# Optimization experiments

Measured on AMD Instinct MI355X. Metric: run time of the kernel, lower is better.

## Reference

```python
import jax, jax.numpy as jnp
import numpy as np

BS, SEQ, D_MODEL, N_HEADS = 4, 2048, 1024, 16
D_HEAD = D_MODEL // N_HEADS


def setup_inputs() -> dict:
    key = jax.random.key(0)
    ks = jax.random.split(key, 12)
    s = 1.0 / np.sqrt(D_MODEL)
    return {
        "Q": jax.random.normal(ks[0], (BS, SEQ, D_MODEL), jnp.float32),
        "K": jax.random.normal(ks[1], (BS, SEQ, D_MODEL), jnp.float32),
        "V": jax.random.normal(ks[2], (BS, SEQ, D_MODEL), jnp.float32),
        "mask": jax.random.randint(ks[3], (BS, 1, 1, SEQ), 0, 2, jnp.int32),
        "Wq": jax.random.normal(ks[4], (D_MODEL, D_MODEL), jnp.float32) * s,
        "bq": jnp.zeros((D_MODEL,), jnp.float32),
        "Wk": jax.random.normal(ks[5], (D_MODEL, D_MODEL), jnp.float32) * s,
        "bk": jnp.zeros((D_MODEL,), jnp.float32),
        "Wv": jax.random.normal(ks[6], (D_MODEL, D_MODEL), jnp.float32) * s,
        "bv": jnp.zeros((D_MODEL,), jnp.float32),
        "Wo": jax.random.normal(ks[7], (D_MODEL, D_MODEL), jnp.float32) * s,
        "bo": jnp.zeros((D_MODEL,), jnp.float32),
    }


def _split_heads(x):
    # (b, s, d_model) -> (b, h, s, d_head)
    b, s, _ = x.shape
    return x.reshape(b, s, N_HEADS, D_HEAD).transpose(0, 2, 1, 3)


def reference(Q, K, V, mask, Wq, bq, Wk, bk, Wv, bv, Wo, bo):
    q = _split_heads(Q @ Wq.T + bq)
    k = _split_heads(K @ Wk.T + bk)
    v = _split_heads(V @ Wv.T + bv)
    # (b, h, sq, sk) score matrix, scaled by sqrt(d_head)
    scores = jnp.einsum("bhqd,bhkd->bhqk", q, k) / np.sqrt(D_HEAD).astype(np.float32)
    scores = jnp.where(mask == 0, jnp.float32(-1e9), scores)
    attn = jax.nn.softmax(scores, axis=-1)
    ctx = jnp.einsum("bhqk,bhkd->bhqd", attn, v)
    b, h, s, d = ctx.shape
    ctx = ctx.transpose(0, 2, 1, 3).reshape(b, s, h * d)
    return ctx @ Wo.T + bo
```

## Files before the change

kernel.cpp:

```cpp
#include <hip/hip_runtime.h>


typedef __attribute__((ext_vector_type(8))) unsigned short us8;
typedef __attribute__((ext_vector_type(4))) unsigned short us4;
typedef __attribute__((ext_vector_type(4))) int i4;
typedef __attribute__((ext_vector_type(4))) float f4;
typedef __attribute__((ext_vector_type(4))) float f32x4;
typedef __attribute__((ext_vector_type(8))) __bf16 bf16x8;
typedef __attribute__((ext_vector_type(2))) unsigned u32x2;
typedef __attribute__((ext_vector_type(4))) unsigned u32x4;

#define DEV static __device__ __forceinline__

DEV unsigned short f2bf(float f){
  unsigned u = __builtin_bit_cast(unsigned, f);
  u = (u + 0x7fffu + ((u >> 16) & 1u)) >> 16;
  return (unsigned short)u;
}

DEV bf16x8 ld_frag(const unsigned short* p){
  return __builtin_bit_cast(bf16x8, *(const us8*)p);
}

DEV void gll16(const unsigned short* gsrc, unsigned short* ldst){
  __builtin_amdgcn_global_load_lds(
      (const __attribute__((address_space(1))) unsigned int*)gsrc,
      (__attribute__((address_space(3))) unsigned int*)ldst, 16, 0, 0);
}

DEV us8 ld_cvt_f32x8(const float* p){
  f4 v0 = *(const f4*)p;
  f4 v1 = *(const f4*)(p + 4);
  unsigned d0, d1, d2, d3;
  asm("v_cvt_pk_bf16_f32 %0, %1, %2" : "=v"(d0) : "v"(v0[0]), "v"(v0[1]));
  asm("v_cvt_pk_bf16_f32 %0, %1, %2" : "=v"(d1) : "v"(v0[2]), "v"(v0[3]));
  asm("v_cvt_pk_bf16_f32 %0, %1, %2" : "=v"(d2) : "v"(v1[0]), "v"(v1[1]));
  asm("v_cvt_pk_bf16_f32 %0, %1, %2" : "=v"(d3) : "v"(v1[2]), "v"(v1[3]));
  u32x4 u = {d0, d1, d2, d3};
  return __builtin_bit_cast(us8, u);
}

__global__ void cvt_bf16x4(const float* __restrict__ w0, const float* __restrict__ w1,
                           const float* __restrict__ w2, const float* __restrict__ w3,
                           unsigned short* __restrict__ o0, unsigned short* __restrict__ o1,
                           unsigned short* __restrict__ o2, unsigned short* __restrict__ o3)
{
  const int z = blockIdx.y;
  const float* src = (z == 0) ? w0 : (z == 1) ? w1 : (z == 2) ? w2 : w3;
  unsigned short* dst = (z == 0) ? o0 : (z == 1) ? o1 : (z == 2) ? o2 : o3;
  int i = blockIdx.x * 256 + threadIdx.x;
  *(us8*)(dst + (size_t)i * 8) = ld_cvt_f32x8(src + (size_t)i * 8);
}

__global__ __launch_bounds__(256) void mask_scan(
    const int* __restrict__ mask, int* __restrict__ idx, int* __restrict__ nk)
{
  const int b = blockIdx.x, t = threadIdx.x;
  __shared__ int sc[256];
  int m[8]; int c = 0;
#pragma unroll
  for(int r = 0; r < 8; ++r){ m[r] = mask[b * 2048 + t * 8 + r]; c += (m[r] != 0); }
  sc[t] = c;
  __syncthreads();
  for(int s = 1; s < 256; s <<= 1){
    int v = (t >= s) ? sc[t - s] : 0;
    __syncthreads();
    sc[t] += v;
    __syncthreads();
  }
  int pos = sc[t] - c;
  int total = sc[255];
#pragma unroll
  for(int r = 0; r < 8; ++r) if(m[r]) idx[b * 2048 + pos++] = t * 8 + r;
  int pend = (total + 127) & ~127;
  for(int p = total + t; p < pend; p += 256) idx[b * 2048 + p] = 0;
  if(t == 0) nk[b] = total;
}

__global__ __launch_bounds__(256) void qkv_proj(
    const float* __restrict__ Qf, const float* __restrict__ Kf, const float* __restrict__ Vf,
    const unsigned short* __restrict__ Wqb, const unsigned short* __restrict__ Wkb,
    const unsigned short* __restrict__ Wvb,
    const float* __restrict__ bq, const float* __restrict__ bk, const float* __restrict__ bv,
    unsigned short* __restrict__ qs, unsigned short* __restrict__ ksc,
    unsigned short* __restrict__ vTc, float qscale,
    const int* __restrict__ gidx, const int* __restrict__ nkarr)
{
  __shared__ __align__(16) unsigned short As[128 * 64];
  __shared__ __align__(16) unsigned short Bs[128 * 64];
  const int tid = threadIdx.x;
  const int x = blockIdx.x, z = blockIdx.y >> 3, ny = blockIdx.y & 7;
  const int w = tid >> 6, l = tid & 63, g = l >> 4, l15 = l & 15;
  const int wm = w >> 1, wn = w & 1;
  const int xsw = ((l & 7) ^ (l >> 3)) << 3;
  const int ch = tid & 7, srow = tid >> 3;

  int ia[4];
  int gb = 0;
  if(z >= 1){
    gb = (x * 128) >> 11;
    const int j0 = (x * 128) & 2047;
    if(j0 >= ((nkarr[gb] + 127) & ~127)) return;
#pragma unroll
    for(int i = 0; i < 4; ++i)
      ia[i] = gidx[gb * 2048 + j0 + srow + i * 32];
  }

  const float*          Af32 = (z == 0) ? Qf : Kf;
  const unsigned short* Wb   = (z == 0) ? Wqb : Wkb;

  f32x4 acc[4][4];
#pragma unroll
  for(int a = 0; a < 4; ++a)
#pragma unroll
    for(int b = 0; b < 4; ++b) acc[a][b] = (f32x4){0.f,0.f,0.f,0.f};

  for(int kt = 0; kt < 16; ++kt){
    __syncthreads();
    if(z < 2){
#pragma unroll
      for(int i = 0; i < 4; ++i){
        int row = srow + i * 32;
        const float* src = (z == 1)
          ? Af32 + ((size_t)gb * 2048 + ia[i]) * 1024 + kt * 64 + ch * 8
          : Af32 + (size_t)(x * 128 + row) * 1024 + kt * 64 + ch * 8;
        us8 va = ld_cvt_f32x8(src);
        *(us8*)&As[row * 64 + ((ch * 8) ^ ((row & 7) << 3))] = va;
      }
#pragma unroll
      for(int j = 0; j < 4; ++j)
        gll16(Wb + (size_t)(ny * 128 + (w << 5) + (j << 3) + (l >> 3)) * 1024 + kt * 64 + xsw,
              &Bs[((w << 5) + (j << 3)) << 6]);
    } else {
#pragma unroll
      for(int j = 0; j < 4; ++j)
        gll16(Wvb + (size_t)(ny * 128 + (w << 5) + (j << 3) + (l >> 3)) * 1024 + kt * 64 + xsw,
              &As[((w << 5) + (j << 3)) << 6]);
#pragma unroll
      for(int i = 0; i < 4; ++i){
        int row = srow + i * 32;
        const float* src = Vf + ((size_t)gb * 2048 + ia[i]) * 1024 + kt * 64 + ch * 8;
        us8 vb = ld_cvt_f32x8(src);
        *(us8*)&Bs[row * 64 + ((ch * 8) ^ ((row & 7) << 3))] = vb;
      }
    }
    asm volatile("s_waitcnt vmcnt(0)" ::: "memory");
    __syncthreads();
#pragma unroll
    for(int kk = 0; kk < 2; ++kk){
      bf16x8 af[4], bg[4];
#pragma unroll
      for(int mi = 0; mi < 4; ++mi){
        int row = wm * 64 + mi * 16 + l15;
        af[mi] = ld_frag(&As[row * 64 + ((kk * 32 + g * 8) ^ ((row & 7) << 3))]);
      }
#pragma unroll
      for(int ni = 0; ni < 4; ++ni){
        int row = wn * 64 + ni * 16 + l15;
        bg[ni] = ld_frag(&Bs[row * 64 + ((kk * 32 + g * 8) ^ ((row & 7) << 3))]);
      }
#pragma unroll
      for(int mi = 0; mi < 4; ++mi)
#pragma unroll
        for(int ni = 0; ni < 4; ++ni)
          acc[mi][ni] = __builtin_amdgcn_mfma_f32_16x16x32_bf16(af[mi], bg[ni], acc[mi][ni], 0, 0, 0);
    }
  }

  if(z < 2){
    const float scale = (z == 0) ? qscale : 1.0f;
    const float* bias = (z == 0) ? bq : bk;
    unsigned short* out = (z == 0) ? qs : ksc;
#pragma unroll
    for(int mi = 0; mi < 4; ++mi)
#pragma unroll
      for(int ni = 0; ni < 4; ++ni){
        int gmb = x * 128 + wm * 64 + mi * 16 + g * 4;
        int gn  = ny * 128 + wn * 64 + ni * 16 + l15;
#pragma unroll
        for(int r = 0; r < 4; ++r){
          int gm = gmb + r;
          float v = (acc[mi][ni][r] + bias[gn]) * scale;
          int b = gm >> 11, s = gm & 2047, h = gn >> 6, dh = gn & 63;
          out[(size_t)(((b << 4) + h) * 2048 + s) * 64 + dh] = f2bf(v);
        }
      }
  } else {
#pragma unroll
    for(int mi = 0; mi < 4; ++mi)
#pragma unroll
      for(int ni = 0; ni < 4; ++ni){
        int gmb = ny * 128 + wm * 64 + mi * 16 + g * 4;
        int gn  = x * 128 + wn * 64 + ni * 16 + l15;
#pragma unroll
        for(int r = 0; r < 4; ++r){
          int gm = gmb + r;
          float v = acc[mi][ni][r] + bv[gm];
          int h = gm >> 6, dh = gm & 63, b = gn >> 11, s = gn & 2047;
          vTc[(size_t)(((b << 4) + h) * 64 + dh) * 2048 + s] = f2bf(v);
        }
      }
  }
}

__global__ __launch_bounds__(256) void gemm_out(
    const unsigned short* __restrict__ Ap, const unsigned short* __restrict__ Bp,
    const float* __restrict__ bias, float* __restrict__ outp, int K)
{
  __shared__ __align__(16) unsigned short As[128 * 64];
  __shared__ __align__(16) unsigned short Bs[128 * 64];
  const int tid = threadIdx.x;
  const int gy = blockIdx.x, gx = blockIdx.y;
  const int w = tid >> 6, l = tid & 63, g = l >> 4, l15 = l & 15;
  const int wm = w >> 1, wn = w & 1;
  const int xsw = ((l & 7) ^ (l >> 3)) << 3;

  f32x4 acc[4][4];
#pragma unroll
  for(int a = 0; a < 4; ++a)
#pragma unroll
    for(int b = 0; b < 4; ++b) acc[a][b] = (f32x4){0.f,0.f,0.f,0.f};

  const int nkt = K >> 6;
  for(int kt = 0; kt < nkt; ++kt){
    __syncthreads();
#pragma unroll
    for(int j = 0; j < 4; ++j)
      gll16(Ap + (size_t)(gy * 128 + (w << 5) + (j << 3) + (l >> 3)) * K + kt * 64 + xsw,
            &As[((w << 5) + (j << 3)) << 6]);
#pragma unroll
    for(int j = 0; j < 4; ++j)
      gll16(Bp + (size_t)(gx * 128 + (w << 5) + (j << 3) + (l >> 3)) * K + kt * 64 + xsw,
            &Bs[((w << 5) + (j << 3)) << 6]);
    asm volatile("s_waitcnt vmcnt(0)" ::: "memory");
    __syncthreads();
#pragma unroll
    for(int kk = 0; kk < 2; ++kk){
      bf16x8 af[4], bg[4];
#pragma unroll
      for(int mi = 0; mi < 4; ++mi){
        int row = wm * 64 + mi * 16 + l15;
        af[mi] = ld_frag(&As[row * 64 + ((kk * 32 + g * 8) ^ ((row & 7) << 3))]);
      }
#pragma unroll
      for(int ni = 0; ni < 4; ++ni){
        int row = wn * 64 + ni * 16 + l15;
        bg[ni] = ld_frag(&Bs[row * 64 + ((kk * 32 + g * 8) ^ ((row & 7) << 3))]);
      }
#pragma unroll
      for(int mi = 0; mi < 4; ++mi)
#pragma unroll
        for(int ni = 0; ni < 4; ++ni)
          acc[mi][ni] = __builtin_amdgcn_mfma_f32_16x16x32_bf16(af[mi], bg[ni], acc[mi][ni], 0, 0, 0);
    }
  }

#pragma unroll
  for(int mi = 0; mi < 4; ++mi)
#pragma unroll
    for(int ni = 0; ni < 4; ++ni){
      int gmb = gy * 128 + wm * 64 + mi * 16 + g * 4;
      int gn  = gx * 128 + wn * 64 + ni * 16 + l15;
#pragma unroll
      for(int r = 0; r < 4; ++r)
        outp[(size_t)(gmb + r) * 1024 + gn] = acc[mi][ni][r] + bias[gn];
    }
}

__global__ __launch_bounds__(256) void attn_kernel(
    const unsigned short* __restrict__ q, const unsigned short* __restrict__ ksc,
    const unsigned short* __restrict__ vTc, const int* __restrict__ nk,
    unsigned short* __restrict__ ctx)
{
  __shared__ __align__(16) unsigned short KsB[2][64 * 64];
  __shared__ __align__(16) unsigned short VtB[2][64 * 64];
  __shared__ __align__(16) unsigned short Ps[4][16 * 64];

  const int bh = blockIdx.x;
  const int qt = blockIdx.y;
  const int b  = bh >> 4, h = bh & 15;
  const int tid = threadIdx.x;
  const int w = tid >> 6, l = tid & 63, g = l >> 4, l15 = l & 15;
  const int rl = l >> 3, c8 = l & 7;

  const int nkb = nk[b];
  const int nt = (nkb + 63) >> 6;

  const unsigned short* qbase = q + ((size_t)(bh * 2048 + qt * 64 + w * 16 + l15)) * 64;
  bf16x8 bq[2];
  bq[0] = ld_frag(qbase + g * 8);
  bq[1] = ld_frag(qbase + 32 + g * 8);

  const unsigned short* kbase = ksc + (size_t)bh * 2048 * 64;
  const unsigned short* vbase = vTc + (size_t)bh * 64 * 2048;

  const unsigned short* kg0 = kbase + (size_t)(w * 16 + rl) * 64 + c8 * 8;
  const unsigned short* vg0 = vbase + (size_t)(w * 16 + rl) * 2048 + c8 * 8;
  const int lo0 = (w * 16 + rl) * 64 + ((c8 ^ rl) << 3);
  const int lo1 = lo0 + 8 * 64;

  us8 kr0, kr1, vr0, vr1;
#define LOAD_T(kt_) do{                                        \
    kr0 = *(const us8*)(kg0 + (size_t)(kt_) * 4096);           \
    kr1 = *(const us8*)(kg0 + (size_t)(kt_) * 4096 + 512);     \
    vr0 = *(const us8*)(vg0 + (size_t)(kt_) * 64);             \
    vr1 = *(const us8*)(vg0 + (size_t)(kt_) * 64 + 8 * 2048);  \
  }while(0)
#define WRITE_T(bb_) do{                                       \
    *(us8*)&KsB[bb_][lo0] = kr0;                               \
    *(us8*)&KsB[bb_][lo1] = kr1;                               \
    *(us8*)&VtB[bb_][lo0] = vr0;                               \
    *(us8*)&VtB[bb_][lo1] = vr1;                               \
  }while(0)

  f32x4 acc[4];
#pragma unroll
  for(int mi = 0; mi < 4; ++mi) acc[mi] = (f32x4){0.f,0.f,0.f,0.f};
  float ll = 0.f;

  LOAD_T(0);
  WRITE_T(0);
  __syncthreads();

  for(int kt = 0; kt < nt; ++kt){
    const int bb = kt & 1;
    if(kt + 1 < nt) LOAD_T(kt + 1);

    f32x4 sa[4];
#pragma unroll
    for(int mi = 0; mi < 4; ++mi) sa[mi] = (f32x4){0.f,0.f,0.f,0.f};
    __builtin_amdgcn_s_setprio(1);
#pragma unroll
    for(int kk = 0; kk < 2; ++kk){
#pragma unroll
      for(int mi = 0; mi < 4; ++mi){
        int row = mi * 16 + l15;
        bf16x8 af = ld_frag(&KsB[bb][row * 64 + ((kk * 32 + g * 8) ^ ((row & 7) << 3))]);
        sa[mi] = __builtin_amdgcn_mfma_f32_16x16x32_bf16(af, bq[kk], sa[mi], 0, 0, 0);
      }
    }
    __builtin_amdgcn_s_setprio(0);

    float p[4][4];
    if((kt + 1) * 64 <= nkb){
#pragma unroll
      for(int mi = 0; mi < 4; ++mi)
#pragma unroll
        for(int r = 0; r < 4; ++r){
          p[mi][r] = __builtin_amdgcn_exp2f(sa[mi][r]);
          ll += p[mi][r];
        }
    } else {
      int kb0 = kt * 64 + g * 4;
#pragma unroll
      for(int mi = 0; mi < 4; ++mi)
#pragma unroll
        for(int r = 0; r < 4; ++r){
          float e = __builtin_amdgcn_exp2f(sa[mi][r]);
          p[mi][r] = (kb0 + mi * 16 + r < nkb) ? e : 0.f;
          ll += p[mi][r];
        }
    }

#pragma unroll
    for(int mi = 0; mi < 4; ++mi){
      unsigned d0, d1;
      asm("v_cvt_pk_bf16_f32 %0, %1, %2" : "=v"(d0) : "v"(p[mi][0]), "v"(p[mi][1]));
      asm("v_cvt_pk_bf16_f32 %0, %1, %2" : "=v"(d1) : "v"(p[mi][2]), "v"(p[mi][3]));
      u32x2 dd = {d0, d1};
      *(u32x2*)&Ps[w][l15 * 64 + ((mi * 16 + g * 4) ^ ((l15 & 7) << 3))] = dd;
    }

    __builtin_amdgcn_s_setprio(1);
#pragma unroll
    for(int kk = 0; kk < 2; ++kk){
      bf16x8 pb = ld_frag(&Ps[w][l15 * 64 + ((kk * 32 + g * 8) ^ ((l15 & 7) << 3))]);
#pragma unroll
      for(int mi = 0; mi < 4; ++mi){
        int row = mi * 16 + l15;
        bf16x8 av = ld_frag(&VtB[bb][row * 64 + ((kk * 32 + g * 8) ^ ((row & 7) << 3))]);
        acc[mi] = __builtin_amdgcn_mfma_f32_16x16x32_bf16(av, pb, acc[mi], 0, 0, 0);
      }
    }
    __builtin_amdgcn_s_setprio(0);

    if(kt + 1 < nt) WRITE_T(bb ^ 1);
    __syncthreads();
  }

  ll += __shfl_xor(ll, 16);
  ll += __shfl_xor(ll, 32);
  float inv = 1.0f / ll;

  {
    int qrow = w * 16 + l15;
#pragma unroll
    for(int mi = 0; mi < 4; ++mi){
      us4 o;
#pragma unroll
      for(int r = 0; r < 4; ++r) o[r] = f2bf(acc[mi][r] * inv);
      *(us4*)&KsB[0][qrow * 64 + ((mi * 16 + g * 4) ^ ((qrow & 7) << 3))] = o;
    }
  }
  __syncthreads();
  {
    int qrow = tid >> 2, part = tid & 3;
    us8 v0 = *(const us8*)&KsB[0][qrow * 64 + ((part * 16)     ^ ((qrow & 7) << 3))];
    us8 v1 = *(const us8*)&KsB[0][qrow * 64 + ((part * 16 + 8) ^ ((qrow & 7) << 3))];
    size_t orow = ((size_t)b * 2048 + qt * 64 + qrow) * 1024 + h * 64 + part * 16;
    *(us8*)&ctx[orow] = v0;
    *(us8*)&ctx[orow + 8] = v1;
  }
#undef LOAD_T
#undef WRITE_T
}

extern "C" void kernel_launch(void* const* d_in, const int* in_sizes, int n_in,
                              void* d_out, int out_size, void* d_ws, size_t ws_size,
                              hipStream_t stream) {
  const float* Qf = (const float*)d_in[0];
  const float* Kf = (const float*)d_in[1];
  const float* Vf = (const float*)d_in[2];
  const int*   Mk = (const int*)d_in[3];
  const float* Wq = (const float*)d_in[4];
  const float* bq = (const float*)d_in[5];
  const float* Wk = (const float*)d_in[6];
  const float* bk = (const float*)d_in[7];
  const float* Wv = (const float*)d_in[8];
  const float* bv = (const float*)d_in[9];
  const float* Wo = (const float*)d_in[10];
  const float* bo = (const float*)d_in[11];

  const size_t MB = 1u << 20;
  char* ws = (char*)d_ws;
  unsigned short* Wqb = (unsigned short*)(ws + 0 * MB);
  unsigned short* Wkb = (unsigned short*)(ws + 2 * MB);
  unsigned short* Wvb = (unsigned short*)(ws + 4 * MB);
  unsigned short* Wob = (unsigned short*)(ws + 6 * MB);
  unsigned short* qs  = (unsigned short*)(ws + 8 * MB);
  unsigned short* ksc = (unsigned short*)(ws + 24 * MB);
  unsigned short* vTc = (unsigned short*)(ws + 40 * MB);
  unsigned short* ctx = (unsigned short*)(ws + 56 * MB);
  int* idx = (int*)(ws + 72 * MB);
  int* nk  = (int*)(ws + 73 * MB);

  mask_scan<<<4, 256, 0, stream>>>(Mk, idx, nk);
  cvt_bf16x4<<<dim3(512, 4), 256, 0, stream>>>(Wq, Wk, Wv, Wo, Wqb, Wkb, Wvb, Wob);

  const float QSCALE = 0.125f * 1.4426950408889634f;
  dim3 blk(256);
  qkv_proj<<<dim3(64, 24), blk, 0, stream>>>(Qf, Kf, Vf, Wqb, Wkb, Wvb,
                                             bq, bk, bv, qs, ksc, vTc, QSCALE,
                                             idx, nk);
  attn_kernel<<<dim3(64, 32), blk, 0, stream>>>(qs, ksc, vTc, nk, ctx);
  gemm_out<<<dim3(64, 8), blk, 0, stream>>>(ctx, Wob, bo, (float*)d_out, 1024);
}
```

Measured before the change: 175.0 us.

## Pre-convert and gather Q/K/V activations to bf16 before projection GEMM

Adds a combined conversion kernel that turns the weights and also the Q, K and V activations into bf16, gathering only unmasked K/V rows into compact buffers. The projection GEMM then loads both operands straight into LDS with global_load_lds, with no per-tile fp32 load and convert in registers. Each fp32 activation tile was being re-read and re-converted by every one of the 8 N-blocks, and this removes that repeated work. The cost is an extra round trip through memory for the bf16 activation copies, about 48MB of extra traffic.

Measured after the change: 173.3 us (median of 2 runs). Within noise of the previous version (-1.0%).

```diff
diff --git a/kernel.cpp b/kernel.cpp
--- a/kernel.cpp
+++ b/kernel.cpp
@@ -40,18 +40,6 @@
   return __builtin_bit_cast(us8, u);
 }
 
-__global__ void cvt_bf16x4(const float* __restrict__ w0, const float* __restrict__ w1,
-                           const float* __restrict__ w2, const float* __restrict__ w3,
-                           unsigned short* __restrict__ o0, unsigned short* __restrict__ o1,
-                           unsigned short* __restrict__ o2, unsigned short* __restrict__ o3)
-{
-  const int z = blockIdx.y;
-  const float* src = (z == 0) ? w0 : (z == 1) ? w1 : (z == 2) ? w2 : w3;
-  unsigned short* dst = (z == 0) ? o0 : (z == 1) ? o1 : (z == 2) ? o2 : o3;
-  int i = blockIdx.x * 256 + threadIdx.x;
-  *(us8*)(dst + (size_t)i * 8) = ld_cvt_f32x8(src + (size_t)i * 8);
-}
-
 __global__ __launch_bounds__(256) void mask_scan(
     const int* __restrict__ mask, int* __restrict__ idx, int* __restrict__ nk)
 {
@@ -77,14 +65,48 @@
   if(t == 0) nk[b] = total;
 }
 
+__global__ __launch_bounds__(256) void cvt_all(
+    const float* __restrict__ Wq, const float* __restrict__ Wk,
+    const float* __restrict__ Wv, const float* __restrict__ Wo,
+    const float* __restrict__ Qf, const float* __restrict__ Kf, const float* __restrict__ Vf,
+    unsigned short* __restrict__ Wqb, unsigned short* __restrict__ Wkb,
+    unsigned short* __restrict__ Wvb, unsigned short* __restrict__ Wob,
+    unsigned short* __restrict__ Qb, unsigned short* __restrict__ Kbc,
+    unsigned short* __restrict__ Vbc,
+    const int* __restrict__ gidx, const int* __restrict__ nkarr)
+{
+  const int y = blockIdx.y, x = blockIdx.x, t = threadIdx.x;
+  if(y < 4){
+    if(x >= 512) return;
+    const float* src = (y == 0) ? Wq : (y == 1) ? Wk : (y == 2) ? Wv : Wo;
+    unsigned short* dst = (y == 0) ? Wqb : (y == 1) ? Wkb : (y == 2) ? Wvb : Wob;
+    size_t i = (size_t)x * 2048 + t * 8;
+    *(us8*)(dst + i) = ld_cvt_f32x8(src + i);
+  } else if(y == 4){
+    size_t i = (size_t)x * 2048 + t * 8;
+    *(us8*)(Qb + i) = ld_cvt_f32x8(Qf + i);
+  } else {
+    const float* src = (y == 5) ? Kf : Vf;
+    unsigned short* dst = (y == 5) ? Kbc : Vbc;
+    int r0 = x * 2;
+    int b = r0 >> 11, j = r0 & 2047;
+    if(j >= ((nkarr[b] + 127) & ~127)) return;
+    int rr = t >> 7;
+    int srow = gidx[b * 2048 + j + rr];
+    int col = (t & 127) * 8;
+    *(us8*)(dst + (size_t)(r0 + rr) * 1024 + col) =
+        ld_cvt_f32x8(src + ((size_t)b * 2048 + srow) * 1024 + col);
+  }
+}
+
 __global__ __launch_bounds__(256) void qkv_proj(
-    const float* __restrict__ Qf, const float* __restrict__ Kf, const float* __restrict__ Vf,
+    const unsigned short* __restrict__ Qb, const unsigned short* __restrict__ Kbc,
+    const unsigned short* __restrict__ Vbc,
     const unsigned short* __restrict__ Wqb, const unsigned short* __restrict__ Wkb,
     const unsigned short* __restrict__ Wvb,
     const float* __restrict__ bq, const float* __restrict__ bk, const float* __restrict__ bv,
     unsigned short* __restrict__ qs, unsigned short* __restrict__ ksc,
-    unsigned short* __restrict__ vTc, float qscale,
-    const int* __restrict__ gidx, const int* __restrict__ nkarr)
+    unsigned short* __restrict__ vTc, float qscale, const int* __restrict__ nkarr)
 {
   __shared__ __align__(16) unsigned short As[128 * 64];
   __shared__ __align__(16) unsigned short Bs[128 * 64];
@@ -93,21 +115,17 @@
   const int w = tid >> 6, l = tid & 63, g = l >> 4, l15 = l & 15;
   const int wm = w >> 1, wn = w & 1;
   const int xsw = ((l & 7) ^ (l >> 3)) << 3;
-  const int ch = tid & 7, srow = tid >> 3;
-
-  int ia[4];
-  int gb = 0;
+
   if(z >= 1){
-    gb = (x * 128) >> 11;
-    const int j0 = (x * 128) & 2047;
+    const int gb = (x * 128) >> 11, j0 = (x * 128) & 2047;
     if(j0 >= ((nkarr[gb] + 127) & ~127)) return;
-#pragma unroll
-    for(int i = 0; i < 4; ++i)
-      ia[i] = gidx[gb * 2048 + j0 + srow + i * 32];
-  }
-
-  const float*          Af32 = (z == 0) ? Qf : Kf;
-  const unsigned short* Wb   = (z == 0) ? Wqb : Wkb;
+  }
+
+  const unsigned short* Ab = (z == 0) ? Qb : (z == 1) ? Kbc : Wvb;
+  const unsigned short* Bb = (z == 0) ? Wqb : (z == 1) ? Wkb : Vbc;
+  const int abase = (z == 2) ? ny * 128 : x * 128;
+  const int bbase = (z == 2) ? x * 128 : ny * 128;
+  const int lrow = (w << 5) + (l >> 3);
 
   f32x4 acc[4][4];
 #pragma unroll
@@ -117,33 +135,14 @@
 
   for(int kt = 0; kt < 16; ++kt){
     __syncthreads();
-    if(z < 2){
-#pragma unroll
-      for(int i = 0; i < 4; ++i){
-        int row = srow + i * 32;
-        const float* src = (z == 1)
-          ? Af32 + ((size_t)gb * 2048 + ia[i]) * 1024 + kt * 64 + ch * 8
-          : Af32 + (size_t)(x * 128 + row) * 1024 + kt * 64 + ch * 8;
-        us8 va = ld_cvt_f32x8(src);
-        *(us8*)&As[row * 64 + ((ch * 8) ^ ((row & 7) << 3))] = va;
-      }
-#pragma unroll
-      for(int j = 0; j < 4; ++j)
-        gll16(Wb + (size_t)(ny * 128 + (w << 5) + (j << 3) + (l >> 3)) * 1024 + kt * 64 + xsw,
-              &Bs[((w << 5) + (j << 3)) << 6]);
-    } else {
-#pragma unroll
-      for(int j = 0; j < 4; ++j)
-        gll16(Wvb + (size_t)(ny * 128 + (w << 5) + (j << 3) + (l >> 3)) * 1024 + kt * 64 + xsw,
-              &As[((w << 5) + (j << 3)) << 6]);
-#pragma unroll
-      for(int i = 0; i < 4; ++i){
-        int row = srow + i * 32;
-        const float* src = Vf + ((size_t)gb * 2048 + ia[i]) * 1024 + kt * 64 + ch * 8;
-        us8 vb = ld_cvt_f32x8(src);
-        *(us8*)&Bs[row * 64 + ((ch * 8) ^ ((row & 7) << 3))] = vb;
-      }
-    }
+#pragma unroll
+    for(int j = 0; j < 4; ++j)
+      gll16(Ab + (size_t)(abase + lrow + (j << 3)) * 1024 + kt * 64 + xsw,
+            &As[((w << 5) + (j << 3)) << 6]);
+#pragma unroll
+    for(int j = 0; j < 4; ++j)
+      gll16(Bb + (size_t)(bbase + lrow + (j << 3)) * 1024 + kt * 64 + xsw,
+            &Bs[((w << 5) + (j << 3)) << 6]);
     asm volatile("s_waitcnt vmcnt(0)" ::: "memory");
     __syncthreads();
 #pragma unroll
@@ -443,15 +442,19 @@
   unsigned short* ctx = (unsigned short*)(ws + 56 * MB);
   int* idx = (int*)(ws + 72 * MB);
   int* nk  = (int*)(ws + 73 * MB);
+  unsigned short* Qb  = (unsigned short*)(ws + 74 * MB);
+  unsigned short* Kbc = (unsigned short*)(ws + 90 * MB);
+  unsigned short* Vbc = (unsigned short*)(ws + 106 * MB);
 
   mask_scan<<<4, 256, 0, stream>>>(Mk, idx, nk);
-  cvt_bf16x4<<<dim3(512, 4), 256, 0, stream>>>(Wq, Wk, Wv, Wo, Wqb, Wkb, Wvb, Wob);
+  cvt_all<<<dim3(4096, 7), 256, 0, stream>>>(Wq, Wk, Wv, Wo, Qf, Kf, Vf,
+                                             Wqb, Wkb, Wvb, Wob, Qb, Kbc, Vbc,
+                                             idx, nk);
 
   const float QSCALE = 0.125f * 1.4426950408889634f;
   dim3 blk(256);
-  qkv_proj<<<dim3(64, 24), blk, 0, stream>>>(Qf, Kf, Vf, Wqb, Wkb, Wvb,
-                                             bq, bk, bv, qs, ksc, vTc, QSCALE,
-                                             idx, nk);
+  qkv_proj<<<dim3(64, 24), blk, 0, stream>>>(Qb, Kbc, Vbc, Wqb, Wkb, Wvb,
+                                             bq, bk, bv, qs, ksc, vTc, QSCALE, nk);
   attn_kernel<<<dim3(64, 32), blk, 0, stream>>>(qs, ksc, vTc, nk, ctx);
   gemm_out<<<dim3(64, 8), blk, 0, stream>>>(ctx, Wob, bo, (float*)d_out, 1024);
 }
```
